# Performance work log

Measured on AMD Instinct MI355X. Metric: run time of the kernel, lower is better.

## Reference

```python
import jax, jax.numpy as jnp
import numpy as np
from jax import lax

K = 16  # neighbors (includes self, as PyG DynamicEdgeConv's knn(x, x, k) does)


def _knn_idx(pts):
    # pts: [n, d] -> [n, K] indices of K nearest points (incl. self)
    sq = jnp.sum(pts * pts, axis=-1)
    dist = sq[:, None] + sq[None, :] - 2.0 * (pts @ pts.T)  # [n, n]
    _, idx = lax.top_k(-dist, K)
    return idx


def _edge_conv(x, w1, b1, w2, b2):
    # x: [B, n, d]. Dynamic kNN in feature space, per-edge MLP, max-aggregation.
    idx = jax.vmap(_knn_idx)(x)                      # [B, n, K]
    xj = jax.vmap(lambda xb, ib: xb[ib])(x, idx)     # [B, n, K, d]
    xi = x[:, :, None, :]
    e = jnp.concatenate([jnp.broadcast_to(xi, xj.shape), xj - xi], axis=-1)  # [B,n,K,2d]
    h = jax.nn.relu(e @ w1 + b1)                     # [B, n, K, h]
    h = h @ w2 + b2                                  # plain last layer (PyG MLP plain_last)
    return jnp.max(h, axis=2)                        # max aggr over neighbors -> [B, n, h]


def setup_inputs() -> dict:
    key = jax.random.key(0)
    ks = jax.random.split(key, 16)
    B, n = 64, 1024
    c1, c2, c3 = 64, 64, 64
    m1, m2, m3, oc = 128, 64, 32, 2

    def lin(k, i, o):
        s = 1.0 / np.sqrt(i)
        return jax.random.uniform(k, (i, o), jnp.float32, -s, s)

    inp = {
        "x": jax.random.normal(ks[0], (B, n, 1), jnp.float32),
        "c1w1": lin(ks[1], 2, c1),   "c1b1": jnp.zeros((c1,), jnp.float32),
        "c1w2": lin(ks[2], c1, c1),  "c1b2": jnp.zeros((c1,), jnp.float32),
        "c2w1": lin(ks[3], 2 * c1, c2), "c2b1": jnp.zeros((c2,), jnp.float32),
        "c2w2": lin(ks[4], c2, c2),  "c2b2": jnp.zeros((c2,), jnp.float32),
        "c3w1": lin(ks[5], 2 * c2, c3), "c3b1": jnp.zeros((c3,), jnp.float32),
        "c3w2": lin(ks[6], c3, c3),  "c3b2": jnp.zeros((c3,), jnp.float32),
        "mw1": lin(ks[7], c1 + c2 + c3, m1), "mb1": jnp.zeros((m1,), jnp.float32),
        "mw2": lin(ks[8], m1, m2),   "mb2": jnp.zeros((m2,), jnp.float32),
        "mw3": lin(ks[9], m2, m3),   "mb3": jnp.zeros((m3,), jnp.float32),
        "mw4": lin(ks[10], m3, oc),  "mb4": jnp.zeros((oc,), jnp.float32),
    }
    return inp


def reference(x, c1w1, c1b1, c1w2, c1b2, c2w1, c2b1, c2w2, c2b2,
              c3w1, c3b1, c3w2, c3b2, mw1, mb1, mw2, mb2, mw3, mb3, mw4, mb4):
    # Three DynamicEdgeConv layers (eval mode: batch-norms are identity at init, dropout off)
    x1 = _edge_conv(x, c1w1, c1b1, c1w2, c1b2)   # [B, n, 64]
    x2 = _edge_conv(x1, c2w1, c2b1, c2w2, c2b2)  # [B, n, 64]
    x3 = _edge_conv(x2, c3w1, c3b1, c3w2, c3b2)  # [B, n, 64]
    h = jnp.concatenate([x1, x2, x3], axis=-1)   # [B, n, 192]
    h = jax.nn.relu(h @ mw1 + mb1)
    h = jax.nn.relu(h @ mw2 + mb2)
    h = jax.nn.relu(h @ mw3 + mb3)
    out = h @ mw4 + mb4                          # [B, n, 2]
    return jax.nn.log_softmax(out, axis=-1)
```

## Files before the change

### kernel.cpp

```cpp
#include <hip/hip_runtime.h>
#include <math.h>

typedef unsigned short ushort_t;
typedef unsigned int uint_t;
typedef unsigned long long u64_t;
typedef __bf16 bf16x8_t __attribute__((ext_vector_type(8)));
typedef float f32x4_t __attribute__((ext_vector_type(4)));

static constexpr int NPTS = 1024;
static constexpr int NB = 64;
static constexpr int NPOINTS = NB * NPTS;
static constexpr int KNB = 16;

__device__ __forceinline__ ushort_t f2bf(float f) {
    uint_t u = __float_as_uint(f);
    uint_t r = (u + 0x7FFFu + ((u >> 16) & 1u)) >> 16;
    return (ushort_t)r;
}
__device__ __forceinline__ uint_t packdj(float d, int j) {
    return (__float_as_uint(fmaxf(d, 0.f)) & 0xFFFFFC00u) | (uint_t)j;
}
__device__ __forceinline__ uint_t med3u(uint_t a, uint_t b, uint_t c) {
    uint_t d;
    asm("v_med3_u32 %0, %1, %2, %3" : "=v"(d) : "v"(a), "v"(b), "v"(c));
    return d;
}
__device__ __forceinline__ void insert16(uint_t* L, uint_t c) {
    #pragma unroll
    for (int k = 15; k > 0; --k)
        L[k] = med3u(L[k - 1], L[k], c);
    L[0] = L[0] < c ? L[0] : c;
}
__device__ __forceinline__ uint_t f2ord(float f) {
    uint_t u = __float_as_uint(f);
    return (u & 0x80000000u) ? ~u : (u ^ 0x80000000u);
}

__global__ __launch_bounds__(256) void prep_kernel(const float* __restrict__ mw1,
                                                   const float* __restrict__ c1w2,
                                                   const float* __restrict__ c2w2,
                                                   const float* __restrict__ c3w2,
                                                   const float* __restrict__ c1w1,
                                                   const float* __restrict__ c1b1,
                                                   const float* __restrict__ c2w1,
                                                   const float* __restrict__ c3w1,
                                                   const float* __restrict__ mw2,
                                                   const float* __restrict__ mw3,
                                                   ushort_t* __restrict__ w1fh,
                                                   ushort_t* __restrict__ w1fl,
                                                   ushort_t* __restrict__ w2fh,
                                                   ushort_t* __restrict__ w2fl,
                                                   float* __restrict__ wuv,
                                                   ushort_t* __restrict__ wuvfh,
                                                   ushort_t* __restrict__ wuvfl,
                                                   ushort_t* __restrict__ w23fh,
                                                   ushort_t* __restrict__ w23fl) {
    int blk = blockIdx.x;
    if (blk < 96) {
        int t = blk * 256 + threadIdx.x;
        int e = t & 7;
        int lane = (t >> 3) & 63;
        int fs = t >> 9;
        int nt = fs / 6, ks = fs - nt * 6;
        int m = lane & 15, quad = lane >> 4;
        int k = ks * 32 + quad * 8 + e;
        int n = nt * 16 + m;
        float w = mw1[k * 128 + n];
        uint_t bits = __float_as_uint(w);
        float hif = __uint_as_float(bits & 0xFFFF0000u);
        w1fh[t] = (ushort_t)(bits >> 16);
        w1fl[t] = f2bf(w - hif);
    } else if (blk < 144) {
        int layer = (blk - 96) >> 4;
        const float* w2 = layer == 0 ? c1w2 : (layer == 1 ? c2w2 : c3w2);
        int t = ((blk - 96) & 15) * 256 + threadIdx.x;
        int e = t & 7;
        int lane = (t >> 3) & 63;
        int fs = t >> 9;
        int ct = fs >> 1, kh = fs & 1;
        int m = lane & 15, quad = lane >> 4;
        int k = kh * 32 + quad * 8 + e;
        int n = ct * 16 + m;
        float w = w2[k * 64 + n];
        uint_t bits = __float_as_uint(w);
        float hif = __uint_as_float(bits & 0xFFFF0000u);
        w2fh[layer * 4096 + t] = (ushort_t)(bits >> 16);
        w2fl[layer * 4096 + t] = f2bf(w - hif);
    } else if (blk == 144) {
        for (int s = threadIdx.x; s < 3072; s += 256) {
            int arr = s >> 10, r = s & 1023;
            int lane = r >> 4, ce = r & 15;
            int kh = ce >> 3, e = ce & 7;
            int quad = lane >> 4;
            int c = kh * 32 + quad * 8 + e;
            float val = (arr == 0) ? (c1w1[c] - c1w1[64 + c])
                      : (arr == 1) ? c1w1[64 + c] : c1b1[c];
            wuv[s] = val;
        }
    } else if (blk < 209) {
        int layer = (blk - 145) >> 5;
        const float* w1 = layer == 0 ? c2w1 : c3w1;
        int t = ((blk - 145) & 31) * 256 + threadIdx.x;
        int e = t & 7;
        int lane = (t >> 3) & 63;
        int fs = t >> 9;
        int nt = fs >> 1, ks = fs & 1;
        int m = lane & 15, quad = lane >> 4;
        int k = ks * 32 + quad * 8 + e;
        float w;
        if (nt < 4) {
            int n = nt * 16 + m;
            w = w1[k * 64 + n] - w1[(64 + k) * 64 + n];
        } else {
            int n = (nt - 4) * 16 + m;
            w = w1[(64 + k) * 64 + n];
        }
        uint_t bits = __float_as_uint(w);
        float hif = __uint_as_float(bits & 0xFFFF0000u);
        wuvfh[layer * 8192 + t] = (ushort_t)(bits >> 16);
        wuvfl[layer * 8192 + t] = f2bf(w - hif);
    } else if (blk < 241) {
        int t = (blk - 209) * 256 + threadIdx.x;
        int e = t & 7;
        int lane = (t >> 3) & 63;
        int fs = t >> 9;
        int nt = fs >> 2, ks = fs & 3;
        int m = lane & 15, quad = lane >> 4;
        int k = ks * 32 + quad * 8 + e;
        int n = nt * 16 + m;
        float w = mw2[k * 64 + n];
        uint_t bits = __float_as_uint(w);
        float hif = __uint_as_float(bits & 0xFFFF0000u);
        w23fh[t] = (ushort_t)(bits >> 16);
        w23fl[t] = f2bf(w - hif);
    } else {
        int t = (blk - 241) * 256 + threadIdx.x;
        int e = t & 7;
        int lane = (t >> 3) & 63;
        int fs = t >> 9;
        int nt = fs >> 1, ks = fs & 1;
        int m = lane & 15, quad = lane >> 4;
        int k = ks * 32 + quad * 8 + e;
        int n = nt * 16 + m;
        float w = mw3[k * 32 + n];
        uint_t bits = __float_as_uint(w);
        float hif = __uint_as_float(bits & 0xFFFF0000u);
        w23fh[8192 + t] = (ushort_t)(bits >> 16);
        w23fl[8192 + t] = f2bf(w - hif);
    }
}

__global__ __launch_bounds__(256) void knn1_sort_kernel(const float* __restrict__ pts,
                                                        int* __restrict__ idx_out) {
    __shared__ u64_t keys[NPTS];
    int b = blockIdx.x;
    int t = threadIdx.x;
    const float* base = pts + (size_t)b * NPTS;
    for (int s = t; s < NPTS; s += 256)
        keys[s] = ((u64_t)f2ord(base[s]) << 32) | (uint_t)s;
    for (int k = 2; k <= NPTS; k <<= 1) {
        for (int j2 = k >> 1; j2 > 0; j2 >>= 1) {
            __syncthreads();
            for (int i = t; i < NPTS; i += 256) {
                int ix = i ^ j2;
                if (ix > i) {
                    bool asc = ((i & k) == 0);
                    u64_t a = keys[i], c = keys[ix];
                    if ((a > c) == asc) { keys[i] = c; keys[ix] = a; }
                }
            }
        }
    }
    __syncthreads();
    for (int s = t; s < NPTS; s += 256) {
        u64_t me = keys[s];
        int jme = (int)(me & 0x3FFu);
        uint_t mo = (uint_t)(me >> 32);
        uint_t mu = (mo & 0x80000000u) ? (mo ^ 0x80000000u) : ~mo;
        float xs = __uint_as_float(mu);
        uint_t lst[KNB];
        #pragma unroll
        for (int k = 0; k < KNB; ++k) lst[k] = 0xFFFFFFFFu;
        int lo = s - 16; if (lo < 0) lo = 0;
        int hi = s + 16; if (hi > NPTS - 1) hi = NPTS - 1;
        for (int q = lo; q <= hi; ++q) {
            u64_t o = keys[q];
            uint_t oo = (uint_t)(o >> 32);
            uint_t ou = (oo & 0x80000000u) ? (oo ^ 0x80000000u) : ~oo;
            float xo = __uint_as_float(ou);
            float d = (xs - xo) * (xs - xo);
            insert16(lst, packdj(d, (int)(o & 0x3FFu)));
        }
        int* op = idx_out + ((size_t)b * NPTS + jme) * KNB;
        #pragma unroll
        for (int k = 0; k < KNB; ++k) op[k] = (int)(lst[k] & 0x3FFu);
    }
}

__global__ __launch_bounds__(256, 4) void knn_mfma_kernel(const ushort_t* __restrict__ xh,
                                                          const ushort_t* __restrict__ xl,
                                                          const float* __restrict__ sq,
                                                          int* __restrict__ idx_out) {
    constexpr int JC = NPTS / 4;
    __shared__ uint_t dmem[4][1088];
    int b    = blockIdx.x & 63;
    int ib   = blockIdx.x >> 6;
    int wave = threadIdx.x >> 6;
    int lane = threadIdx.x & 63;
    int i0   = b * NPTS + ib * 64;
    int m = lane & 15, quad = lane >> 4;
    int j0c = wave * JC;
    uint_t* dbuf = dmem[wave];

    bf16x8_t Ah[4][2], Al[4][2];
    #pragma unroll
    for (int it = 0; it < 4; ++it) {
        #pragma unroll
        for (int kh = 0; kh < 2; ++kh) {
            size_t off = ((size_t)(i0 + it * 16 + m)) * 64 + kh * 32 + quad * 8;
            Ah[it][kh] = *(const bf16x8_t*)(xh + off);
            Al[it][kh] = *(const bf16x8_t*)(xl + off);
        }
    }
    float4 sqi[4];
    #pragma unroll
    for (int it = 0; it < 4; ++it)
        sqi[it] = *(const float4*)&sq[i0 + it * 16 + quad * 4];

    uint_t lst[KNB];
    #pragma unroll
    for (int k = 0; k < KNB; ++k) lst[k] = 0xFFFFFFFFu;

    for (int g = 0; g < JC / 16; ++g) {
        int jg = j0c + g * 16;
        size_t boff = ((size_t)(b * NPTS + jg + m)) * 64 + quad * 8;
        bf16x8_t Bh0 = *(const bf16x8_t*)(xh + boff);
        bf16x8_t Bh1 = *(const bf16x8_t*)(xh + boff + 32);
        bf16x8_t Bl0 = *(const bf16x8_t*)(xl + boff);
        bf16x8_t Bl1 = *(const bf16x8_t*)(xl + boff + 32);
        float sqj = sq[b * NPTS + jg + m];
        int jm = jg + m;
        #pragma unroll
        for (int it = 0; it < 4; ++it) {
            f32x4_t acc = {0.f, 0.f, 0.f, 0.f};
            acc = __builtin_amdgcn_mfma_f32_16x16x32_bf16(Ah[it][0], Bh0, acc, 0, 0, 0);
            acc = __builtin_amdgcn_mfma_f32_16x16x32_bf16(Ah[it][1], Bh1, acc, 0, 0, 0);
            acc = __builtin_amdgcn_mfma_f32_16x16x32_bf16(Ah[it][0], Bl0, acc, 0, 0, 0);
            acc = __builtin_amdgcn_mfma_f32_16x16x32_bf16(Ah[it][1], Bl1, acc, 0, 0, 0);
            acc = __builtin_amdgcn_mfma_f32_16x16x32_bf16(Al[it][0], Bh0, acc, 0, 0, 0);
            acc = __builtin_amdgcn_mfma_f32_16x16x32_bf16(Al[it][1], Bh1, acc, 0, 0, 0);
            uint4 pv;
            pv.x = packdj(sqi[it].x + sqj - 2.0f * acc[0], jm);
            pv.y = packdj(sqi[it].y + sqj - 2.0f * acc[1], jm);
            pv.z = packdj(sqi[it].z + sqj - 2.0f * acc[2], jm);
            pv.w = packdj(sqi[it].w + sqj - 2.0f * acc[3], jm);
            *(uint4*)&dbuf[m * 68 + it * 16 + quad * 4] = pv;
        }
        #pragma unroll
        for (int jj = 0; jj < 16; ++jj)
            insert16(lst, dbuf[jj * 68 + lane]);
    }
    #pragma unroll
    for (int k = 0; k < KNB; ++k) dmem[wave][lane * 17 + k] = lst[k];
    __syncthreads();
    if (wave == 0) {
        uint_t fin[KNB];
        #pragma unroll
        for (int k = 0; k < KNB; ++k) fin[k] = 0xFFFFFFFFu;
        #pragma unroll
        for (int c = 0; c < 4; ++c)
            #pragma unroll
            for (int k = 0; k < KNB; ++k)
                insert16(fin, dmem[c][lane * 17 + k]);
        int* op = idx_out + (size_t)(i0 + lane) * KNB;
        #pragma unroll
        for (int k = 0; k < KNB; ++k) op[k] = (int)(fin[k] & 0x3FFu);
    }
}

__global__ __launch_bounds__(256) void uv_mfma_kernel(const ushort_t* __restrict__ xh,
                                                      const ushort_t* __restrict__ xl,
                                                      const ushort_t* __restrict__ wufh,
                                                      const ushort_t* __restrict__ wufl,
                                                      const float* __restrict__ b1,
                                                      float* __restrict__ u,
                                                      float* __restrict__ v) {
    int wave = threadIdx.x >> 6, lane = threadIdx.x & 63;
    int m = lane & 15, quad = lane >> 4;
    int b = blockIdx.x & 63;
    int r = blockIdx.x >> 6;
    int p0 = b * NPTS + r * 64 + wave * 16;
    bf16x8_t Ah[2], Al[2];
    #pragma unroll
    for (int ks = 0; ks < 2; ++ks) {
        size_t aoff = (size_t)(p0 + m) * 64 + ks * 32 + quad * 8;
        Ah[ks] = *(const bf16x8_t*)(xh + aoff);
        Al[ks] = *(const bf16x8_t*)(xl + aoff);
    }
    f32x4_t acc[8];
    #pragma unroll
    for (int nt = 0; nt < 8; ++nt) acc[nt] = (f32x4_t){0.f, 0.f, 0.f, 0.f};
    #pragma unroll
    for (int ks = 0; ks < 2; ++ks) {
        #pragma unroll
        for (int nt = 0; nt < 8; ++nt) {
            size_t boff = (size_t)((nt * 2 + ks) * 64 + lane) * 8;
            bf16x8_t Bh = *(const bf16x8_t*)(wufh + boff);
            bf16x8_t Bl = *(const bf16x8_t*)(wufl + boff);
            acc[nt] = __builtin_amdgcn_mfma_f32_16x16x32_bf16(Ah[ks], Bh, acc[nt], 0, 0, 0);
            acc[nt] = __builtin_amdgcn_mfma_f32_16x16x32_bf16(Ah[ks], Bl, acc[nt], 0, 0, 0);
            acc[nt] = __builtin_amdgcn_mfma_f32_16x16x32_bf16(Al[ks], Bh, acc[nt], 0, 0, 0);
        }
    }
    #pragma unroll
    for (int nt = 0; nt < 8; ++nt) {
        int ch = (nt & 3) * 16 + m;
        float bb = (nt < 4) ? b1[ch] : 0.f;
        float* dst = (nt < 4) ? u : v;
        #pragma unroll
        for (int rr = 0; rr < 4; ++rr) {
            int p = p0 + quad * 4 + rr;
            dst[(size_t)p * 64 + ch] = acc[nt][rr] + bb;
        }
    }
}

__global__ __launch_bounds__(256) void edge1_mfma_kernel(const float* __restrict__ x0,
                                                         const int* __restrict__ idx,
                                                         const ushort_t* __restrict__ w2fh,
                                                         const ushort_t* __restrict__ w2fl,
                                                         const float* __restrict__ wuv,
                                                         const float* __restrict__ b2,
                                                         ushort_t* __restrict__ oh,
                                                         ushort_t* __restrict__ ol,
                                                         float* __restrict__ sqout) {
    int wave = threadIdx.x >> 6, lane = threadIdx.x & 63;
    int m = lane & 15, quad = lane >> 4;
    bf16x8_t Bh[4][2], Bl[4][2];
    #pragma unroll
    for (int ct = 0; ct < 4; ++ct) {
        #pragma unroll
        for (int kh = 0; kh < 2; ++kh) {
            size_t boff = (size_t)((ct * 2 + kh) * 64 + lane) * 8;
            Bh[ct][kh] = *(const bf16x8_t*)(w2fh + boff);
            Bl[ct][kh] = *(const bf16x8_t*)(w2fl + boff);
        }
    }
    float wdv[16], wbv[16], bbv[16];
    #pragma unroll
    for (int q = 0; q < 4; ++q) {
        *(float4*)&wdv[q * 4] = *(const float4*)&wuv[lane * 16 + q * 4];
        *(float4*)&wbv[q * 4] = *(const float4*)&wuv[1024 + lane * 16 + q * 4];
        *(float4*)&bbv[q * 4] = *(const float4*)&wuv[2048 + lane * 16 + q * 4];
    }
    float bias[4];
    #pragma unroll
    for (int ct = 0; ct < 4; ++ct) bias[ct] = b2[ct * 16 + m];
    int bb_ = blockIdx.x & 63;
    int r_  = blockIdx.x >> 6;
    int p0 = bb_ * NPTS + r_ * 16 + wave * 4;
    int jv[4];
    #pragma unroll
    for (int pi = 0; pi < 4; ++pi) jv[pi] = idx[(p0 + pi) * 16 + m];
    float xj4[4];
    #pragma unroll
    for (int pi = 0; pi < 4; ++pi) xj4[pi] = x0[(bb_ << 10) + jv[pi]];
    #pragma unroll
    for (int pi = 0; pi < 4; ++pi) {
        int p = p0 + pi;
        float xi = x0[p];
        float xj = xj4[pi];
        bf16x8_t Ah[2], Al[2];
        #pragma unroll
        for (int kh = 0; kh < 2; ++kh) {
            union { ushort_t s[8]; bf16x8_t v8; } H, L;
            #pragma unroll
            for (int e = 0; e < 8; ++e) {
                int ce = kh * 8 + e;
                float g = fmaxf(fmaf(xi, wdv[ce], fmaf(xj, wbv[ce], bbv[ce])), 0.f);
                uint_t bits = __float_as_uint(g);
                H.s[e] = (ushort_t)(bits >> 16);
                float hif = __uint_as_float(bits & 0xFFFF0000u);
                L.s[e] = (ushort_t)(__float_as_uint(g - hif) >> 16);
            }
            Ah[kh] = H.v8; Al[kh] = L.v8;
        }
        float val[4];
        #pragma unroll
        for (int ct = 0; ct < 4; ++ct) {
            f32x4_t acc = {0.f, 0.f, 0.f, 0.f};
            acc = __builtin_amdgcn_mfma_f32_16x16x32_bf16(Ah[0], Bh[ct][0], acc, 0, 0, 0);
            acc = __builtin_amdgcn_mfma_f32_16x16x32_bf16(Ah[1], Bh[ct][1], acc, 0, 0, 0);
            acc = __builtin_amdgcn_mfma_f32_16x16x32_bf16(Ah[0], Bl[ct][0], acc, 0, 0, 0);
            acc = __builtin_amdgcn_mfma_f32_16x16x32_bf16(Ah[1], Bl[ct][1], acc, 0, 0, 0);
            acc = __builtin_amdgcn_mfma_f32_16x16x32_bf16(Al[0], Bh[ct][0], acc, 0, 0, 0);
            acc = __builtin_amdgcn_mfma_f32_16x16x32_bf16(Al[1], Bh[ct][1], acc, 0, 0, 0);
            float mm = fmaxf(fmaxf(acc[0], acc[1]), fmaxf(acc[2], acc[3]));
            mm = fmaxf(mm, __shfl_xor(mm, 16, 64));
            mm = fmaxf(mm, __shfl_xor(mm, 32, 64));
            val[ct] = mm + bias[ct];
        }
        {
            float partial = val[0] * val[0] + val[1] * val[1]
                          + val[2] * val[2] + val[3] * val[3];
            partial += __shfl_xor(partial, 1, 64);
            partial += __shfl_xor(partial, 2, 64);
            partial += __shfl_xor(partial, 4, 64);
            partial += __shfl_xor(partial, 8, 64);
            if (lane == 0) sqout[p] = partial;
        }
        if (quad == 0) {
            #pragma unroll
            for (int ct = 0; ct < 4; ++ct) {
                int o = ct * 16 + m;
                float vv = val[ct];
                uint_t bits = __float_as_uint(vv);
                oh[(size_t)p * 64 + o] = (ushort_t)(bits >> 16);
                float hif = __uint_as_float(bits & 0xFFFF0000u);
                ol[(size_t)p * 64 + o] = f2bf(vv - hif);
            }
        }
    }
}

template<bool WSQ>
__global__ __launch_bounds__(256) void edge_mfma_kernel(const float* __restrict__ u,
                                                        const float* __restrict__ v,
                                                        const int* __restrict__ idx,
                                                        const ushort_t* __restrict__ w2fh,
                                                        const ushort_t* __restrict__ w2fl,
                                                        const float* __restrict__ b2,
                                                        ushort_t* __restrict__ oh,
                                                        ushort_t* __restrict__ ol,
                                                        float* __restrict__ sqout) {
    int wave = threadIdx.x >> 6, lane = threadIdx.x & 63;
    int m = lane & 15, quad = lane >> 4;
    bf16x8_t Bh[4][2], Bl[4][2];
    #pragma unroll
    for (int ct = 0; ct < 4; ++ct) {
        #pragma unroll
        for (int kh = 0; kh < 2; ++kh) {
            size_t boff = (size_t)((ct * 2 + kh) * 64 + lane) * 8;
            Bh[ct][kh] = *(const bf16x8_t*)(w2fh + boff);
            Bl[ct][kh] = *(const bf16x8_t*)(w2fl + boff);
        }
    }
    float bias[4];
    #pragma unroll
    for (int ct = 0; ct < 4; ++ct) bias[ct] = b2[ct * 16 + m];
    int bb_ = blockIdx.x & 63;
    int r_  = blockIdx.x >> 6;
    int p0 = bb_ * NPTS + r_ * 16 + wave * 4;
    int jv[4];
    #pragma unroll
    for (int pi = 0; pi < 4; ++pi) jv[pi] = idx[(p0 + pi) * 16 + m];
    #pragma unroll
    for (int pi = 0; pi < 4; ++pi) {
        int p = p0 + pi;
        const float* up = u + (size_t)p * 64;
        const float* vp = v + ((size_t)(bb_ << 10) + jv[pi]) * 64;
        bf16x8_t Ah[2], Al[2];
        #pragma unroll
        for (int kh = 0; kh < 2; ++kh) {
            int c0 = kh * 32 + quad * 8;
            float4 ua = *(const float4*)(up + c0);
            float4 ub = *(const float4*)(up + c0 + 4);
            float4 va = *(const float4*)(vp + c0);
            float4 vb = *(const float4*)(vp + c0 + 4);
            float f[8] = {ua.x + va.x, ua.y + va.y, ua.z + va.z, ua.w + va.w,
                          ub.x + vb.x, ub.y + vb.y, ub.z + vb.z, ub.w + vb.w};
            union { ushort_t s[8]; bf16x8_t v8; } H, L;
            #pragma unroll
            for (int e = 0; e < 8; ++e) {
                float g = fmaxf(f[e], 0.f);
                uint_t bits = __float_as_uint(g);
                H.s[e] = (ushort_t)(bits >> 16);
                float hif = __uint_as_float(bits & 0xFFFF0000u);
                L.s[e] = (ushort_t)(__float_as_uint(g - hif) >> 16);
            }
            Ah[kh] = H.v8; Al[kh] = L.v8;
        }
        float val[4];
        #pragma unroll
        for (int ct = 0; ct < 4; ++ct) {
            f32x4_t acc = {0.f, 0.f, 0.f, 0.f};
            acc = __builtin_amdgcn_mfma_f32_16x16x32_bf16(Ah[0], Bh[ct][0], acc, 0, 0, 0);
            acc = __builtin_amdgcn_mfma_f32_16x16x32_bf16(Ah[1], Bh[ct][1], acc, 0, 0, 0);
            acc = __builtin_amdgcn_mfma_f32_16x16x32_bf16(Ah[0], Bl[ct][0], acc, 0, 0, 0);
            acc = __builtin_amdgcn_mfma_f32_16x16x32_bf16(Ah[1], Bl[ct][1], acc, 0, 0, 0);
            acc = __builtin_amdgcn_mfma_f32_16x16x32_bf16(Al[0], Bh[ct][0], acc, 0, 0, 0);
            acc = __builtin_amdgcn_mfma_f32_16x16x32_bf16(Al[1], Bh[ct][1], acc, 0, 0, 0);
            float mm = fmaxf(fmaxf(acc[0], acc[1]), fmaxf(acc[2], acc[3]));
            mm = fmaxf(mm, __shfl_xor(mm, 16, 64));
            mm = fmaxf(mm, __shfl_xor(mm, 32, 64));
            val[ct] = mm + bias[ct];
        }
        if constexpr (WSQ) {
            float partial = val[0] * val[0] + val[1] * val[1]
                          + val[2] * val[2] + val[3] * val[3];
            partial += __shfl_xor(partial, 1, 64);
            partial += __shfl_xor(partial, 2, 64);
            partial += __shfl_xor(partial, 4, 64);
            partial += __shfl_xor(partial, 8, 64);
            if (lane == 0) sqout[p] = partial;
        }
        if (quad == 0) {
            #pragma unroll
            for (int ct = 0; ct < 4; ++ct) {
                int o = ct * 16 + m;
                float vv = val[ct];
                uint_t bits = __float_as_uint(vv);
                oh[(size_t)p * 64 + o] = (ushort_t)(bits >> 16);
                float hif = __uint_as_float(bits & 0xFFFF0000u);
                ol[(size_t)p * 64 + o] = f2bf(vv - hif);
            }
        }
    }
}

__global__ __launch_bounds__(128, 2) void mlp_kernel(const ushort_t* __restrict__ xh1,
                                                  const ushort_t* __restrict__ xl1,
                                                  const ushort_t* __restrict__ xh2,
                                                  const ushort_t* __restrict__ xl2,
                                                  const ushort_t* __restrict__ xh3,
                                                  const ushort_t* __restrict__ xl3,
                                                  const ushort_t* __restrict__ w1fh,
                                                  const ushort_t* __restrict__ w1fl,
                                                  const ushort_t* __restrict__ w23fh,
                                                  const ushort_t* __restrict__ w23fl,
                                                  const float* __restrict__ mb1,
                                                  const float* __restrict__ mb2,
                                                  const float* __restrict__ mb3,
                                                  const float* __restrict__ mw4, const float* __restrict__ mb4,
                                                  float* __restrict__ out) {
    __shared__ float smem[2][128 * 17];
    int wave = threadIdx.x >> 6, lane = threadIdx.x & 63;
    float* h1w = smem[wave];
    float* h2w = smem[wave];
    float* h3w = smem[wave] + 64 * 17;
    int m = lane & 15, quad = lane >> 4;
    int pw = blockIdx.x * 32 + wave * 16;

    const ushort_t* HS[3] = {xh1, xh2, xh3};
    const ushort_t* LS[3] = {xl1, xl2, xl3};
    bf16x8_t Ah[6], Al[6];
    #pragma unroll
    for (int ks = 0; ks < 6; ++ks) {
        size_t aoff = (size_t)(pw + m) * 64 + (ks & 1) * 32 + quad * 8;
        Ah[ks] = *(const bf16x8_t*)(HS[ks >> 1] + aoff);
        Al[ks] = *(const bf16x8_t*)(LS[ks >> 1] + aoff);
    }
    f32x4_t acc1[8];
    #pragma unroll
    for (int nt = 0; nt < 8; ++nt) acc1[nt] = (f32x4_t){0.f, 0.f, 0.f, 0.f};
    #pragma unroll
    for (int ks = 0; ks < 6; ++ks) {
        bf16x8_t Bh[8], Bl[8];
        #pragma unroll
        for (int nt = 0; nt < 8; ++nt) {
            size_t boff = (size_t)(nt * 6 + ks) * 512 + lane * 8;
            Bh[nt] = *(const bf16x8_t*)(w1fh + boff);
            Bl[nt] = *(const bf16x8_t*)(w1fl + boff);
        }
        #pragma unroll
        for (int nt = 0; nt < 8; ++nt) {
            acc1[nt] = __builtin_amdgcn_mfma_f32_16x16x32_bf16(Ah[ks], Bh[nt], acc1[nt], 0, 0, 0);
            acc1[nt] = __builtin_amdgcn_mfma_f32_16x16x32_bf16(Ah[ks], Bl[nt], acc1[nt], 0, 0, 0);
            acc1[nt] = __builtin_amdgcn_mfma_f32_16x16x32_bf16(Al[ks], Bh[nt], acc1[nt], 0, 0, 0);
        }
    }
    #pragma unroll
    for (int nt = 0; nt < 8; ++nt) {
        float bb = mb1[nt * 16 + m];
        float4 w;
        w.x = fmaxf(acc1[nt][0] + bb, 0.f);
        w.y = fmaxf(acc1[nt][1] + bb, 0.f);
        w.z = fmaxf(acc1[nt][2] + bb, 0.f);
        w.w = fmaxf(acc1[nt][3] + bb, 0.f);
        *(float4*)&h1w[(nt * 16 + m) * 17 + quad * 4] = w;
    }
    f32x4_t acc2[4];
    #pragma unroll
    for (int nt = 0; nt < 4; ++nt) acc2[nt] = (f32x4_t){0.f, 0.f, 0.f, 0.f};
    #pragma unroll
    for (int ks = 0; ks < 4; ++ks) {
        union { ushort_t s[8]; bf16x8_t v8; } H, L;
        #pragma unroll
        for (int e = 0; e < 8; ++e) {
            float g = h1w[(ks * 32 + quad * 8 + e) * 17 + m];
            uint_t bits = __float_as_uint(g);
            H.s[e] = (ushort_t)(bits >> 16);
            float hif = __uint_as_float(bits & 0xFFFF0000u);
            L.s[e] = f2bf(g - hif);
        }
        bf16x8_t A2h = H.v8, A2l = L.v8;
        #pragma unroll
        for (int nt = 0; nt < 4; ++nt) {
            size_t boff = (size_t)(nt * 4 + ks) * 512 + lane * 8;
            bf16x8_t Bh = *(const bf16x8_t*)(w23fh + boff);
            bf16x8_t Bl = *(const bf16x8_t*)(w23fl + boff);
            acc2[nt] = __builtin_amdgcn_mfma_f32_16x16x32_bf16(A2h, Bh, acc2[nt], 0, 0, 0);
            acc2[nt] = __builtin_amdgcn_mfma_f32_16x16x32_bf16(A2h, Bl, acc2[nt], 0, 0, 0);
            acc2[nt] = __builtin_amdgcn_mfma_f32_16x16x32_bf16(A2l, Bh, acc2[nt], 0, 0, 0);
        }
    }
    #pragma unroll
    for (int nt = 0; nt < 4; ++nt) {
        float bb = mb2[nt * 16 + m];
        float4 w;
        w.x = fmaxf(acc2[nt][0] + bb, 0.f);
        w.y = fmaxf(acc2[nt][1] + bb, 0.f);
        w.z = fmaxf(acc2[nt][2] + bb, 0.f);
        w.w = fmaxf(acc2[nt][3] + bb, 0.f);
        *(float4*)&h2w[(nt * 16 + m) * 17 + quad * 4] = w;
    }
    f32x4_t acc3[2];
    #pragma unroll
    for (int nt = 0; nt < 2; ++nt) acc3[nt] = (f32x4_t){0.f, 0.f, 0.f, 0.f};
    #pragma unroll
    for (int ks = 0; ks < 2; ++ks) {
        union { ushort_t s[8]; bf16x8_t v8; } H, L;
        #pragma unroll
        for (int e = 0; e < 8; ++e) {
            float g = h2w[(ks * 32 + quad * 8 + e) * 17 + m];
            uint_t bits = __float_as_uint(g);
            H.s[e] = (ushort_t)(bits >> 16);
            float hif = __uint_as_float(bits & 0xFFFF0000u);
            L.s[e] = f2bf(g - hif);
        }
        bf16x8_t A3h = H.v8, A3l = L.v8;
        #pragma unroll
        for (int nt = 0; nt < 2; ++nt) {
            size_t boff = (size_t)(8192 + (nt * 2 + ks) * 512) + lane * 8;
            bf16x8_t Bh = *(const bf16x8_t*)(w23fh + boff);
            bf16x8_t Bl = *(const bf16x8_t*)(w23fl + boff);
            acc3[nt] = __builtin_amdgcn_mfma_f32_16x16x32_bf16(A3h, Bh, acc3[nt], 0, 0, 0);
            acc3[nt] = __builtin_amdgcn_mfma_f32_16x16x32_bf16(A3h, Bl, acc3[nt], 0, 0, 0);
            acc3[nt] = __builtin_amdgcn_mfma_f32_16x16x32_bf16(A3l, Bh, acc3[nt], 0, 0, 0);
        }
    }
    #pragma unroll
    for (int nt = 0; nt < 2; ++nt) {
        float bb = mb3[nt * 16 + m];
        float4 w;
        w.x = fmaxf(acc3[nt][0] + bb, 0.f);
        w.y = fmaxf(acc3[nt][1] + bb, 0.f);
        w.z = fmaxf(acc3[nt][2] + bb, 0.f);
        w.w = fmaxf(acc3[nt][3] + bb, 0.f);
        *(float4*)&h3w[(nt * 16 + m) * 17 + quad * 4] = w;
    }
    if (lane < 16) {
        float z0 = mb4[0], z1 = mb4[1];
        #pragma unroll 8
        for (int c = 0; c < 32; ++c) {
            float h = h3w[c * 17 + lane];
            z0 = fmaf(h, mw4[c * 2 + 0], z0);
            z1 = fmaf(h, mw4[c * 2 + 1], z1);
        }
        float mx = fmaxf(z0, z1);
        float ls = mx + logf(expf(z0 - mx) + expf(z1 - mx));
        float2 o; o.x = z0 - ls; o.y = z1 - ls;
        *(float2*)&out[(size_t)(pw + lane) * 2] = o;
    }
}

extern "C" void kernel_launch(void* const* d_in, const int* in_sizes, int n_in,
                              void* d_out, int out_size, void* d_ws, size_t ws_size,
                              hipStream_t stream) {
    const float* x0   = (const float*)d_in[0];
    const float* c1w1 = (const float*)d_in[1];  const float* c1b1 = (const float*)d_in[2];
    const float* c1w2 = (const float*)d_in[3];  const float* c1b2 = (const float*)d_in[4];
    const float* c2w1 = (const float*)d_in[5];  const float* c2b1 = (const float*)d_in[6];
    const float* c2w2 = (const float*)d_in[7];  const float* c2b2 = (const float*)d_in[8];
    const float* c3w1 = (const float*)d_in[9];  const float* c3b1 = (const float*)d_in[10];
    const float* c3w2 = (const float*)d_in[11]; const float* c3b2 = (const float*)d_in[12];
    const float* mw1  = (const float*)d_in[13]; const float* mb1  = (const float*)d_in[14];
    const float* mw2  = (const float*)d_in[15]; const float* mb2  = (const float*)d_in[16];
    const float* mw3  = (const float*)d_in[17]; const float* mb3  = (const float*)d_in[18];
    const float* mw4  = (const float*)d_in[19]; const float* mb4  = (const float*)d_in[20];

    float* ws = (float*)d_ws;
    const size_t NF = (size_t)NPOINTS * 64;
    float* u  = ws;
    float* v  = u + NF;
    float* sq = v + NF;
    int*  idx = (int*)(sq + NPOINTS);
    ushort_t* xh1 = (ushort_t*)(idx + (size_t)NPOINTS * KNB);
    ushort_t* xl1 = xh1 + NF;
    ushort_t* xh2 = xl1 + NF;
    ushort_t* xl2 = xh2 + NF;
    ushort_t* xh3 = xl2 + NF;
    ushort_t* xl3 = xh3 + NF;
    ushort_t* w1fh = xl3 + NF;
    ushort_t* w1fl = w1fh + 128 * 192;
    ushort_t* w2fh = w1fl + 128 * 192;
    ushort_t* w2fl = w2fh + 3 * 4096;
    float* wuv = (float*)(w2fl + 3 * 4096);
    ushort_t* wuvfh = (ushort_t*)(wuv + 3072);
    ushort_t* wuvfl = wuvfh + 2 * 8192;
    ushort_t* w23fh = wuvfl + 2 * 8192;
    ushort_t* w23fl = w23fh + 10240;
    float* out = (float*)d_out;

    prep_kernel<<<249, 256, 0, stream>>>(mw1, c1w2, c2w2, c3w2, c1w1, c1b1,
                                         c2w1, c3w1, mw2, mw3,
                                         w1fh, w1fl, w2fh, w2fl,
                                         wuv, wuvfh, wuvfl, w23fh, w23fl);
    knn1_sort_kernel<<<NB, 256, 0, stream>>>(x0, idx);
    edge1_mfma_kernel<<<NB * 64, 256, 0, stream>>>(
        x0, idx, w2fh, w2fl, wuv, c1b2, xh1, xl1, sq);
    knn_mfma_kernel<<<NB * 16, 256, 0, stream>>>(xh1, xl1, sq, idx);
    uv_mfma_kernel<<<NB * 16, 256, 0, stream>>>(xh1, xl1, wuvfh, wuvfl, c2b1, u, v);
    edge_mfma_kernel<true><<<NPOINTS / 16, 256, 0, stream>>>(
        u, v, idx, w2fh + 4096, w2fl + 4096, c2b2, xh2, xl2, sq);
    knn_mfma_kernel<<<NB * 16, 256, 0, stream>>>(xh2, xl2, sq, idx);
    uv_mfma_kernel<<<NB * 16, 256, 0, stream>>>(xh2, xl2, wuvfh + 8192, wuvfl + 8192,
                                                c3b1, u, v);
    edge_mfma_kernel<false><<<NPOINTS / 16, 256, 0, stream>>>(
        u, v, idx, w2fh + 8192, w2fl + 8192, c3b2, xh3, xl3, nullptr);
    mlp_kernel<<<NPOINTS / 32, 128, 0, stream>>>(xh1, xl1, xh2, xl2, xh3, xl3,
                                                 w1fh, w1fl, w23fh, w23fl,
                                                 mb1, mb2, mb3, mw4, mb4, out);
}
```

Before: 485.9 us.

## Split kNN candidate range across two blocks and merge partial top-16 lists

The kNN kernel now splits the 1024 candidate points of each query tile across two blocks (512 each) and doubles the grid, so more blocks run concurrently and each wave's serial insertion loop is half as long. Each block writes its packed partial top-16 keys to a scratch buffer, and a new merge kernel combines the two lists per point into the final indices. It also stages squared norms in shared memory. The costs are an extra launch, extra global traffic for the partial lists, and a duplicated per-block final merge. The scratch buffer sits after the existing workspace, which assumes that allocation is large enough.

```diff
diff --git a/kernel.cpp b/kernel.cpp
--- a/kernel.cpp
+++ b/kernel.cpp
@@ -200,17 +200,22 @@
 __global__ __launch_bounds__(256, 4) void knn_mfma_kernel(const ushort_t* __restrict__ xh,
                                                           const ushort_t* __restrict__ xl,
                                                           const float* __restrict__ sq,
-                                                          int* __restrict__ idx_out) {
-    constexpr int JC = NPTS / 4;
+                                                          uint_t* __restrict__ pout) {
+    constexpr int JC = 128;
     __shared__ uint_t dmem[4][1088];
+    __shared__ float sqs[4][JC];
     int b    = blockIdx.x & 63;
-    int ib   = blockIdx.x >> 6;
+    int r    = blockIdx.x >> 6;
+    int ib   = r & 15;
+    int jh   = r >> 4;
     int wave = threadIdx.x >> 6;
     int lane = threadIdx.x & 63;
     int i0   = b * NPTS + ib * 64;
     int m = lane & 15, quad = lane >> 4;
-    int j0c = wave * JC;
+    int j0c = jh * 512 + wave * JC;
     uint_t* dbuf = dmem[wave];
+
+    for (int t = lane; t < JC; t += 64) sqs[wave][t] = sq[b * NPTS + j0c + t];
 
     bf16x8_t Ah[4][2], Al[4][2];
     #pragma unroll
@@ -238,7 +243,7 @@
         bf16x8_t Bh1 = *(const bf16x8_t*)(xh + boff + 32);
         bf16x8_t Bl0 = *(const bf16x8_t*)(xl + boff);
         bf16x8_t Bl1 = *(const bf16x8_t*)(xl + boff + 32);
-        float sqj = sq[b * NPTS + jg + m];
+        float sqj = sqs[wave][g * 16 + m];
         int jm = jg + m;
         #pragma unroll
         for (int it = 0; it < 4; ++it) {
@@ -272,10 +277,33 @@
             #pragma unroll
             for (int k = 0; k < KNB; ++k)
                 insert16(fin, dmem[c][lane * 17 + k]);
-        int* op = idx_out + (size_t)(i0 + lane) * KNB;
-        #pragma unroll
-        for (int k = 0; k < KNB; ++k) op[k] = (int)(fin[k] & 0x3FFu);
-    }
+        uint_t* op = pout + ((size_t)jh * NPOINTS + i0 + lane) * KNB;
+        #pragma unroll
+        for (int k = 0; k < KNB; ++k) op[k] = fin[k];
+    }
+}
+
+__global__ __launch_bounds__(256) void knn_merge_kernel(const uint_t* __restrict__ pknn,
+                                                        int* __restrict__ idx_out) {
+    int p = blockIdx.x * 256 + threadIdx.x;
+    union { uint4 v[4]; uint_t s[16]; } A, B;
+    const uint4* ap = (const uint4*)(pknn + (size_t)p * KNB);
+    const uint4* bp = (const uint4*)(pknn + ((size_t)NPOINTS + p) * KNB);
+    #pragma unroll
+    for (int q = 0; q < 4; ++q) A.v[q] = ap[q];
+    #pragma unroll
+    for (int q = 0; q < 4; ++q) B.v[q] = bp[q];
+    uint_t lst[KNB];
+    #pragma unroll
+    for (int k = 0; k < KNB; ++k) lst[k] = A.s[k];
+    #pragma unroll
+    for (int k = 0; k < KNB; ++k) insert16(lst, B.s[k]);
+    union { int4 v[4]; int s[16]; } O;
+    #pragma unroll
+    for (int k = 0; k < KNB; ++k) O.s[k] = (int)(lst[k] & 0x3FFu);
+    int4* op = (int4*)(idx_out + (size_t)p * KNB);
+    #pragma unroll
+    for (int q = 0; q < 4; ++q) op[q] = O.v[q];
 }
 
 __global__ __launch_bounds__(256) void uv_mfma_kernel(const ushort_t* __restrict__ xh,
@@ -700,6 +728,7 @@
     ushort_t* wuvfl = wuvfh + 2 * 8192;
     ushort_t* w23fh = wuvfl + 2 * 8192;
     ushort_t* w23fl = w23fh + 10240;
+    uint_t* pknn = (uint_t*)(w23fl + 10240);
     float* out = (float*)d_out;
 
     prep_kernel<<<249, 256, 0, stream>>>(mw1, c1w2, c2w2, c3w2, c1w1, c1b1,
@@ -709,11 +738,13 @@
     knn1_sort_kernel<<<NB, 256, 0, stream>>>(x0, idx);
     edge1_mfma_kernel<<<NB * 64, 256, 0, stream>>>(
         x0, idx, w2fh, w2fl, wuv, c1b2, xh1, xl1, sq);
-    knn_mfma_kernel<<<NB * 16, 256, 0, stream>>>(xh1, xl1, sq, idx);
+    knn_mfma_kernel<<<NB * 32, 256, 0, stream>>>(xh1, xl1, sq, pknn);
+    knn_merge_kernel<<<NPOINTS / 256, 256, 0, stream>>>(pknn, idx);
     uv_mfma_kernel<<<NB * 16, 256, 0, stream>>>(xh1, xl1, wuvfh, wuvfl, c2b1, u, v);
     edge_mfma_kernel<true><<<NPOINTS / 16, 256, 0, stream>>>(
         u, v, idx, w2fh + 4096, w2fl + 4096, c2b2, xh2, xl2, sq);
-    knn_mfma_kernel<<<NB * 16, 256, 0, stream>>>(xh2, xl2, sq, idx);
+    knn_mfma_kernel<<<NB * 32, 256, 0, stream>>>(xh2, xl2, sq, pknn);
+    knn_merge_kernel<<<NPOINTS / 256, 256, 0, stream>>>(pknn, idx);
     uv_mfma_kernel<<<NB * 16, 256, 0, stream>>>(xh2, xl2, wuvfh + 8192, wuvfl + 8192,
                                                 c3b1, u, v);
     edge_mfma_kernel<false><<<NPOINTS / 16, 256, 0, stream>>>(
```

Result: slower. 506.8 us (+4.3%).

## Restructure kNN MFMA kernel: per-wave query rows, register top-k with shuffle merge

Applied to the files above, without the earlier changes.

Each wave now owns 16 query points and sweeps all 1024 candidates, swapping MFMA operand roles so every lane holds four distances for its own query row. Lanes insert those distances straight into a register top-16 list instead of going through the shared-memory transpose buffer. The four lane-groups' partial lists are then merged with xor shuffles instead of a block-level LDS merge and __syncthreads. This removes LDS traffic and the barrier, at the cost of more global loads of candidate rows per wave and more insert16 calls per lane.

```diff
diff --git a/kernel.cpp b/kernel.cpp
--- a/kernel.cpp
+++ b/kernel.cpp
@@ -201,80 +201,72 @@
                                                           const ushort_t* __restrict__ xl,
                                                           const float* __restrict__ sq,
                                                           int* __restrict__ idx_out) {
-    constexpr int JC = NPTS / 4;
-    __shared__ uint_t dmem[4][1088];
     int b    = blockIdx.x & 63;
-    int ib   = blockIdx.x >> 6;
+    int r    = blockIdx.x >> 6;
     int wave = threadIdx.x >> 6;
     int lane = threadIdx.x & 63;
-    int i0   = b * NPTS + ib * 64;
     int m = lane & 15, quad = lane >> 4;
-    int j0c = wave * JC;
-    uint_t* dbuf = dmem[wave];
-
-    bf16x8_t Ah[4][2], Al[4][2];
-    #pragma unroll
-    for (int it = 0; it < 4; ++it) {
-        #pragma unroll
-        for (int kh = 0; kh < 2; ++kh) {
-            size_t off = ((size_t)(i0 + it * 16 + m)) * 64 + kh * 32 + quad * 8;
-            Ah[it][kh] = *(const bf16x8_t*)(xh + off);
-            Al[it][kh] = *(const bf16x8_t*)(xl + off);
-        }
-    }
-    float4 sqi[4];
-    #pragma unroll
-    for (int it = 0; it < 4; ++it)
-        sqi[it] = *(const float4*)&sq[i0 + it * 16 + quad * 4];
+    int it = r * 4 + wave;
+    int i0 = b * NPTS + it * 16;
+
+    bf16x8_t Bih[2], Bil[2];
+    #pragma unroll
+    for (int kh = 0; kh < 2; ++kh) {
+        size_t off = (size_t)(i0 + m) * 64 + kh * 32 + quad * 8;
+        Bih[kh] = *(const bf16x8_t*)(xh + off);
+        Bil[kh] = *(const bf16x8_t*)(xl + off);
+    }
+    float sqi = sq[i0 + m];
 
     uint_t lst[KNB];
     #pragma unroll
     for (int k = 0; k < KNB; ++k) lst[k] = 0xFFFFFFFFu;
 
-    for (int g = 0; g < JC / 16; ++g) {
-        int jg = j0c + g * 16;
-        size_t boff = ((size_t)(b * NPTS + jg + m)) * 64 + quad * 8;
-        bf16x8_t Bh0 = *(const bf16x8_t*)(xh + boff);
-        bf16x8_t Bh1 = *(const bf16x8_t*)(xh + boff + 32);
-        bf16x8_t Bl0 = *(const bf16x8_t*)(xl + boff);
-        bf16x8_t Bl1 = *(const bf16x8_t*)(xl + boff + 32);
-        float sqj = sq[b * NPTS + jg + m];
-        int jm = jg + m;
-        #pragma unroll
-        for (int it = 0; it < 4; ++it) {
-            f32x4_t acc = {0.f, 0.f, 0.f, 0.f};
-            acc = __builtin_amdgcn_mfma_f32_16x16x32_bf16(Ah[it][0], Bh0, acc, 0, 0, 0);
-            acc = __builtin_amdgcn_mfma_f32_16x16x32_bf16(Ah[it][1], Bh1, acc, 0, 0, 0);
-            acc = __builtin_amdgcn_mfma_f32_16x16x32_bf16(Ah[it][0], Bl0, acc, 0, 0, 0);
-            acc = __builtin_amdgcn_mfma_f32_16x16x32_bf16(Ah[it][1], Bl1, acc, 0, 0, 0);
-            acc = __builtin_amdgcn_mfma_f32_16x16x32_bf16(Al[it][0], Bh0, acc, 0, 0, 0);
-            acc = __builtin_amdgcn_mfma_f32_16x16x32_bf16(Al[it][1], Bh1, acc, 0, 0, 0);
-            uint4 pv;
-            pv.x = packdj(sqi[it].x + sqj - 2.0f * acc[0], jm);
-            pv.y = packdj(sqi[it].y + sqj - 2.0f * acc[1], jm);
-            pv.z = packdj(sqi[it].z + sqj - 2.0f * acc[2], jm);
-            pv.w = packdj(sqi[it].w + sqj - 2.0f * acc[3], jm);
-            *(uint4*)&dbuf[m * 68 + it * 16 + quad * 4] = pv;
-        }
-        #pragma unroll
-        for (int jj = 0; jj < 16; ++jj)
-            insert16(lst, dbuf[jj * 68 + lane]);
-    }
-    #pragma unroll
-    for (int k = 0; k < KNB; ++k) dmem[wave][lane * 17 + k] = lst[k];
-    __syncthreads();
-    if (wave == 0) {
-        uint_t fin[KNB];
-        #pragma unroll
-        for (int k = 0; k < KNB; ++k) fin[k] = 0xFFFFFFFFu;
-        #pragma unroll
-        for (int c = 0; c < 4; ++c)
-            #pragma unroll
-            for (int k = 0; k < KNB; ++k)
-                insert16(fin, dmem[c][lane * 17 + k]);
-        int* op = idx_out + (size_t)(i0 + lane) * KNB;
-        #pragma unroll
-        for (int k = 0; k < KNB; ++k) op[k] = (int)(fin[k] & 0x3FFu);
+    #pragma unroll 2
+    for (int g = 0; g < 64; ++g) {
+        int jg = g * 16;
+        size_t aoff = (size_t)(b * NPTS + jg + m) * 64 + quad * 8;
+        bf16x8_t Ah0 = *(const bf16x8_t*)(xh + aoff);
+        bf16x8_t Ah1 = *(const bf16x8_t*)(xh + aoff + 32);
+        bf16x8_t Al0 = *(const bf16x8_t*)(xl + aoff);
+        bf16x8_t Al1 = *(const bf16x8_t*)(xl + aoff + 32);
+        float4 sqj = *(const float4*)&sq[b * NPTS + jg + quad * 4];
+        f32x4_t acc = {0.f, 0.f, 0.f, 0.f};
+        acc = __builtin_amdgcn_mfma_f32_16x16x32_bf16(Ah0, Bih[0], acc, 0, 0, 0);
+        acc = __builtin_amdgcn_mfma_f32_16x16x32_bf16(Ah1, Bih[1], acc, 0, 0, 0);
+        acc = __builtin_amdgcn_mfma_f32_16x16x32_bf16(Ah0, Bil[0], acc, 0, 0, 0);
+        acc = __builtin_amdgcn_mfma_f32_16x16x32_bf16(Ah1, Bil[1], acc, 0, 0, 0);
+        acc = __builtin_amdgcn_mfma_f32_16x16x32_bf16(Al0, Bih[0], acc, 0, 0, 0);
+        acc = __builtin_amdgcn_mfma_f32_16x16x32_bf16(Al1, Bih[1], acc, 0, 0, 0);
+        int j0 = jg + quad * 4;
+        insert16(lst, packdj(fmaf(-2.0f, acc[0], sqi + sqj.x), j0));
+        insert16(lst, packdj(fmaf(-2.0f, acc[1], sqi + sqj.y), j0 + 1));
+        insert16(lst, packdj(fmaf(-2.0f, acc[2], sqi + sqj.z), j0 + 2));
+        insert16(lst, packdj(fmaf(-2.0f, acc[3], sqi + sqj.w), j0 + 3));
+    }
+    uint_t tmp[KNB];
+    #pragma unroll
+    for (int k = 0; k < KNB; ++k) tmp[k] = __shfl_xor(lst[k], 16, 64);
+    #pragma unroll
+    for (int k = 0; k < KNB; ++k) insert16(lst, tmp[k]);
+    #pragma unroll
+    for (int k = 0; k < KNB; ++k) tmp[k] = __shfl_xor(lst[k], 32, 64);
+    #pragma unroll
+    for (int k = 0; k < KNB; ++k) insert16(lst, tmp[k]);
+    if (quad == 0) {
+        int* op = idx_out + (size_t)(i0 + m) * KNB;
+        int4 o0 = {(int)(lst[0] & 0x3FFu), (int)(lst[1] & 0x3FFu),
+                   (int)(lst[2] & 0x3FFu), (int)(lst[3] & 0x3FFu)};
+        int4 o1 = {(int)(lst[4] & 0x3FFu), (int)(lst[5] & 0x3FFu),
+                   (int)(lst[6] & 0x3FFu), (int)(lst[7] & 0x3FFu)};
+        int4 o2 = {(int)(lst[8] & 0x3FFu), (int)(lst[9] & 0x3FFu),
+                   (int)(lst[10] & 0x3FFu), (int)(lst[11] & 0x3FFu)};
+        int4 o3 = {(int)(lst[12] & 0x3FFu), (int)(lst[13] & 0x3FFu),
+                   (int)(lst[14] & 0x3FFu), (int)(lst[15] & 0x3FFu)};
+        *(int4*)(op + 0)  = o0;
+        *(int4*)(op + 4)  = o1;
+        *(int4*)(op + 8)  = o2;
+        *(int4*)(op + 12) = o3;
     }
 }
 
```

Result: slower. 601.9 us (+23.9%).

## Fuse kNN and UV projection into one launch; merge partial top-k lists bitonically

Applied to the files above, without the earlier changes.

The kNN and u/v projection kernels become a single launch in which even blocks do kNN and odd blocks do the projection. This removes a kernel launch per layer and lets the lightweight projection blocks fill gaps while the heavy kNN blocks run. The kNN path now stages squared norms of the candidate points in shared memory. The final reduction of the four per-wave top-16 lists uses a bitonic merge instead of 64 serial insertions. Mixing roles in one grid may give uneven block scheduling, and the extra shared memory could affect occupancy.

```diff
diff --git a/kernel.cpp b/kernel.cpp
--- a/kernel.cpp
+++ b/kernel.cpp
@@ -30,6 +30,24 @@
     for (int k = 15; k > 0; --k)
         L[k] = med3u(L[k - 1], L[k], c);
     L[0] = L[0] < c ? L[0] : c;
+}
+__device__ __forceinline__ void merge16(uint_t* L, const uint_t* B) {
+    uint_t t[16];
+    #pragma unroll
+    for (int k = 0; k < 16; ++k) t[k] = L[k] < B[15 - k] ? L[k] : B[15 - k];
+    #pragma unroll
+    for (int j = 8; j >= 1; j >>= 1) {
+        #pragma unroll
+        for (int k = 0; k < 16; ++k) {
+            if ((k & j) == 0) {
+                uint_t a = t[k], c = t[k | j];
+                t[k] = a < c ? a : c;
+                t[k | j] = a < c ? c : a;
+            }
+        }
+    }
+    #pragma unroll
+    for (int k = 0; k < 16; ++k) L[k] = t[k];
 }
 __device__ __forceinline__ uint_t f2ord(float f) {
     uint_t u = __float_as_uint(f);
@@ -197,130 +215,132 @@
     }
 }
 
-__global__ __launch_bounds__(256, 4) void knn_mfma_kernel(const ushort_t* __restrict__ xh,
-                                                          const ushort_t* __restrict__ xl,
-                                                          const float* __restrict__ sq,
-                                                          int* __restrict__ idx_out) {
-    constexpr int JC = NPTS / 4;
+__global__ __launch_bounds__(256, 4) void knnuv_kernel(const ushort_t* __restrict__ xh,
+                                                       const ushort_t* __restrict__ xl,
+                                                       const float* __restrict__ sq,
+                                                       int* __restrict__ idx_out,
+                                                       const ushort_t* __restrict__ wufh,
+                                                       const ushort_t* __restrict__ wufl,
+                                                       const float* __restrict__ b1,
+                                                       float* __restrict__ u,
+                                                       float* __restrict__ v) {
     __shared__ uint_t dmem[4][1088];
-    int b    = blockIdx.x & 63;
-    int ib   = blockIdx.x >> 6;
+    __shared__ float sqs[4][256];
+    int role = blockIdx.x & 1;
+    int id   = blockIdx.x >> 1;
     int wave = threadIdx.x >> 6;
     int lane = threadIdx.x & 63;
-    int i0   = b * NPTS + ib * 64;
     int m = lane & 15, quad = lane >> 4;
-    int j0c = wave * JC;
-    uint_t* dbuf = dmem[wave];
-
-    bf16x8_t Ah[4][2], Al[4][2];
-    #pragma unroll
-    for (int it = 0; it < 4; ++it) {
-        #pragma unroll
-        for (int kh = 0; kh < 2; ++kh) {
-            size_t off = ((size_t)(i0 + it * 16 + m)) * 64 + kh * 32 + quad * 8;
-            Ah[it][kh] = *(const bf16x8_t*)(xh + off);
-            Al[it][kh] = *(const bf16x8_t*)(xl + off);
-        }
-    }
-    float4 sqi[4];
-    #pragma unroll
-    for (int it = 0; it < 4; ++it)
-        sqi[it] = *(const float4*)&sq[i0 + it * 16 + quad * 4];
-
-    uint_t lst[KNB];
-    #pragma unroll
-    for (int k = 0; k < KNB; ++k) lst[k] = 0xFFFFFFFFu;
-
-    for (int g = 0; g < JC / 16; ++g) {
-        int jg = j0c + g * 16;
-        size_t boff = ((size_t)(b * NPTS + jg + m)) * 64 + quad * 8;
-        bf16x8_t Bh0 = *(const bf16x8_t*)(xh + boff);
-        bf16x8_t Bh1 = *(const bf16x8_t*)(xh + boff + 32);
-        bf16x8_t Bl0 = *(const bf16x8_t*)(xl + boff);
-        bf16x8_t Bl1 = *(const bf16x8_t*)(xl + boff + 32);
-        float sqj = sq[b * NPTS + jg + m];
-        int jm = jg + m;
+
+    if (role == 0) {
+        constexpr int JC = NPTS / 4;
+        int b  = id & 63;
+        int ib = id >> 6;
+        int i0 = b * NPTS + ib * 64;
+        int j0c = wave * JC;
+        uint_t* dbuf = dmem[wave];
+
+        for (int t = lane; t < JC; t += 64) sqs[wave][t] = sq[b * NPTS + j0c + t];
+
+        bf16x8_t Ah[4][2], Al[4][2];
         #pragma unroll
         for (int it = 0; it < 4; ++it) {
-            f32x4_t acc = {0.f, 0.f, 0.f, 0.f};
-            acc = __builtin_amdgcn_mfma_f32_16x16x32_bf16(Ah[it][0], Bh0, acc, 0, 0, 0);
-            acc = __builtin_amdgcn_mfma_f32_16x16x32_bf16(Ah[it][1], Bh1, acc, 0, 0, 0);
-            acc = __builtin_amdgcn_mfma_f32_16x16x32_bf16(Ah[it][0], Bl0, acc, 0, 0, 0);
-            acc = __builtin_amdgcn_mfma_f32_16x16x32_bf16(Ah[it][1], Bl1, acc, 0, 0, 0);
-            acc = __builtin_amdgcn_mfma_f32_16x16x32_bf16(Al[it][0], Bh0, acc, 0, 0, 0);
-            acc = __builtin_amdgcn_mfma_f32_16x16x32_bf16(Al[it][1], Bh1, acc, 0, 0, 0);
-            uint4 pv;
-            pv.x = packdj(sqi[it].x + sqj - 2.0f * acc[0], jm);
-            pv.y = packdj(sqi[it].y + sqj - 2.0f * acc[1], jm);
-            pv.z = packdj(sqi[it].z + sqj - 2.0f * acc[2], jm);
-            pv.w = packdj(sqi[it].w + sqj - 2.0f * acc[3], jm);
-            *(uint4*)&dbuf[m * 68 + it * 16 + quad * 4] = pv;
-        }
-        #pragma unroll
-        for (int jj = 0; jj < 16; ++jj)
-            insert16(lst, dbuf[jj * 68 + lane]);
-    }
-    #pragma unroll
-    for (int k = 0; k < KNB; ++k) dmem[wave][lane * 17 + k] = lst[k];
-    __syncthreads();
-    if (wave == 0) {
-        uint_t fin[KNB];
-        #pragma unroll
-        for (int k = 0; k < KNB; ++k) fin[k] = 0xFFFFFFFFu;
-        #pragma unroll
-        for (int c = 0; c < 4; ++c)
-            #pragma unroll
-            for (int k = 0; k < KNB; ++k)
-                insert16(fin, dmem[c][lane * 17 + k]);
-        int* op = idx_out + (size_t)(i0 + lane) * KNB;
-        #pragma unroll
-        for (int k = 0; k < KNB; ++k) op[k] = (int)(fin[k] & 0x3FFu);
-    }
-}
-
-__global__ __launch_bounds__(256) void uv_mfma_kernel(const ushort_t* __restrict__ xh,
-                                                      const ushort_t* __restrict__ xl,
-                                                      const ushort_t* __restrict__ wufh,
-                                                      const ushort_t* __restrict__ wufl,
-                                                      const float* __restrict__ b1,
-                                                      float* __restrict__ u,
-                                                      float* __restrict__ v) {
-    int wave = threadIdx.x >> 6, lane = threadIdx.x & 63;
-    int m = lane & 15, quad = lane >> 4;
-    int b = blockIdx.x & 63;
-    int r = blockIdx.x >> 6;
-    int p0 = b * NPTS + r * 64 + wave * 16;
-    bf16x8_t Ah[2], Al[2];
-    #pragma unroll
-    for (int ks = 0; ks < 2; ++ks) {
-        size_t aoff = (size_t)(p0 + m) * 64 + ks * 32 + quad * 8;
-        Ah[ks] = *(const bf16x8_t*)(xh + aoff);
-        Al[ks] = *(const bf16x8_t*)(xl + aoff);
-    }
-    f32x4_t acc[8];
-    #pragma unroll
-    for (int nt = 0; nt < 8; ++nt) acc[nt] = (f32x4_t){0.f, 0.f, 0.f, 0.f};
-    #pragma unroll
-    for (int ks = 0; ks < 2; ++ks) {
+            #pragma unroll
+            for (int kh = 0; kh < 2; ++kh) {
+                size_t off = ((size_t)(i0 + it * 16 + m)) * 64 + kh * 32 + quad * 8;
+                Ah[it][kh] = *(const bf16x8_t*)(xh + off);
+                Al[it][kh] = *(const bf16x8_t*)(xl + off);
+            }
+        }
+        float4 sqi[4];
+        #pragma unroll
+        for (int it = 0; it < 4; ++it)
+            sqi[it] = *(const float4*)&sq[i0 + it * 16 + quad * 4];
+
+        uint_t lst[KNB];
+        #pragma unroll
+        for (int k = 0; k < KNB; ++k) lst[k] = 0xFFFFFFFFu;
+
+        for (int g = 0; g < JC / 16; ++g) {
+            int jg = j0c + g * 16;
+            size_t boff = ((size_t)(b * NPTS + jg + m)) * 64 + quad * 8;
+            bf16x8_t Bh0 = *(const bf16x8_t*)(xh + boff);
+            bf16x8_t Bh1 = *(const bf16x8_t*)(xh + boff + 32);
+            bf16x8_t Bl0 = *(const bf16x8_t*)(xl + boff);
+            bf16x8_t Bl1 = *(const bf16x8_t*)(xl + boff + 32);
+            float sqj = sqs[wave][g * 16 + m];
+            int jm = jg + m;
+            #pragma unroll
+            for (int it = 0; it < 4; ++it) {
+                f32x4_t acc = {0.f, 0.f, 0.f, 0.f};
+                acc = __builtin_amdgcn_mfma_f32_16x16x32_bf16(Ah[it][0], Bh0, acc, 0, 0, 0);
+                acc = __builtin_amdgcn_mfma_f32_16x16x32_bf16(Ah[it][1], Bh1, acc, 0, 0, 0);
+                acc = __builtin_amdgcn_mfma_f32_16x16x32_bf16(Ah[it][0], Bl0, acc, 0, 0, 0);
+                acc = __builtin_amdgcn_mfma_f32_16x16x32_bf16(Ah[it][1], Bl1, acc, 0, 0, 0);
+                acc = __builtin_amdgcn_mfma_f32_16x16x32_bf16(Al[it][0], Bh0, acc, 0, 0, 0);
+                acc = __builtin_amdgcn_mfma_f32_16x16x32_bf16(Al[it][1], Bh1, acc, 0, 0, 0);
+                uint4 pv;
+                pv.x = packdj(sqi[it].x + sqj - 2.0f * acc[0], jm);
+                pv.y = packdj(sqi[it].y + sqj - 2.0f * acc[1], jm);
+                pv.z = packdj(sqi[it].z + sqj - 2.0f * acc[2], jm);
+                pv.w = packdj(sqi[it].w + sqj - 2.0f * acc[3], jm);
+                *(uint4*)&dbuf[m * 68 + it * 16 + quad * 4] = pv;
+            }
+            #pragma unroll
+            for (int jj = 0; jj < 16; ++jj)
+                insert16(lst, dbuf[jj * 68 + lane]);
+        }
+        #pragma unroll
+        for (int k = 0; k < KNB; ++k) dmem[wave][lane * 17 + k] = lst[k];
+        __syncthreads();
+        if (wave == 0) {
+            uint_t bl[KNB];
+            #pragma unroll
+            for (int c = 1; c < 4; ++c) {
+                #pragma unroll
+                for (int k = 0; k < KNB; ++k) bl[k] = dmem[c][lane * 17 + k];
+                merge16(lst, bl);
+            }
+            int* op = idx_out + (size_t)(i0 + lane) * KNB;
+            #pragma unroll
+            for (int k = 0; k < KNB; ++k) op[k] = (int)(lst[k] & 0x3FFu);
+        }
+    } else {
+        int b = id & 63;
+        int r = id >> 6;
+        int p0 = b * NPTS + r * 64 + wave * 16;
+        bf16x8_t Ah[2], Al[2];
+        #pragma unroll
+        for (int ks = 0; ks < 2; ++ks) {
+            size_t aoff = (size_t)(p0 + m) * 64 + ks * 32 + quad * 8;
+            Ah[ks] = *(const bf16x8_t*)(xh + aoff);
+            Al[ks] = *(const bf16x8_t*)(xl + aoff);
+        }
+        f32x4_t acc[8];
+        #pragma unroll
+        for (int nt = 0; nt < 8; ++nt) acc[nt] = (f32x4_t){0.f, 0.f, 0.f, 0.f};
+        #pragma unroll
+        for (int ks = 0; ks < 2; ++ks) {
+            #pragma unroll
+            for (int nt = 0; nt < 8; ++nt) {
+                size_t boff = (size_t)((nt * 2 + ks) * 64 + lane) * 8;
+                bf16x8_t Bh = *(const bf16x8_t*)(wufh + boff);
+                bf16x8_t Bl = *(const bf16x8_t*)(wufl + boff);
+                acc[nt] = __builtin_amdgcn_mfma_f32_16x16x32_bf16(Ah[ks], Bh, acc[nt], 0, 0, 0);
+                acc[nt] = __builtin_amdgcn_mfma_f32_16x16x32_bf16(Ah[ks], Bl, acc[nt], 0, 0, 0);
+                acc[nt] = __builtin_amdgcn_mfma_f32_16x16x32_bf16(Al[ks], Bh, acc[nt], 0, 0, 0);
+            }
+        }
         #pragma unroll
         for (int nt = 0; nt < 8; ++nt) {
-            size_t boff = (size_t)((nt * 2 + ks) * 64 + lane) * 8;
-            bf16x8_t Bh = *(const bf16x8_t*)(wufh + boff);
-            bf16x8_t Bl = *(const bf16x8_t*)(wufl + boff);
-            acc[nt] = __builtin_amdgcn_mfma_f32_16x16x32_bf16(Ah[ks], Bh, acc[nt], 0, 0, 0);
-            acc[nt] = __builtin_amdgcn_mfma_f32_16x16x32_bf16(Ah[ks], Bl, acc[nt], 0, 0, 0);
-            acc[nt] = __builtin_amdgcn_mfma_f32_16x16x32_bf16(Al[ks], Bh, acc[nt], 0, 0, 0);
-        }
-    }
-    #pragma unroll
-    for (int nt = 0; nt < 8; ++nt) {
-        int ch = (nt & 3) * 16 + m;
-        float bb = (nt < 4) ? b1[ch] : 0.f;
-        float* dst = (nt < 4) ? u : v;
-        #pragma unroll
-        for (int rr = 0; rr < 4; ++rr) {
-            int p = p0 + quad * 4 + rr;
-            dst[(size_t)p * 64 + ch] = acc[nt][rr] + bb;
+            int ch = (nt & 3) * 16 + m;
+            float bb = (nt < 4) ? b1[ch] : 0.f;
+            float* dst = (nt < 4) ? u : v;
+            #pragma unroll
+            for (int rr = 0; rr < 4; ++rr) {
+                int p = p0 + quad * 4 + rr;
+                dst[(size_t)p * 64 + ch] = acc[nt][rr] + bb;
+            }
         }
     }
 }
@@ -709,13 +729,12 @@
     knn1_sort_kernel<<<NB, 256, 0, stream>>>(x0, idx);
     edge1_mfma_kernel<<<NB * 64, 256, 0, stream>>>(
         x0, idx, w2fh, w2fl, wuv, c1b2, xh1, xl1, sq);
-    knn_mfma_kernel<<<NB * 16, 256, 0, stream>>>(xh1, xl1, sq, idx);
-    uv_mfma_kernel<<<NB * 16, 256, 0, stream>>>(xh1, xl1, wuvfh, wuvfl, c2b1, u, v);
+    knnuv_kernel<<<2048, 256, 0, stream>>>(xh1, xl1, sq, idx,
+                                           wuvfh, wuvfl, c2b1, u, v);
     edge_mfma_kernel<true><<<NPOINTS / 16, 256, 0, stream>>>(
         u, v, idx, w2fh + 4096, w2fl + 4096, c2b2, xh2, xl2, sq);
-    knn_mfma_kernel<<<NB * 16, 256, 0, stream>>>(xh2, xl2, sq, idx);
-    uv_mfma_kernel<<<NB * 16, 256, 0, stream>>>(xh2, xl2, wuvfh + 8192, wuvfl + 8192,
-                                                c3b1, u, v);
+    knnuv_kernel<<<2048, 256, 0, stream>>>(xh2, xl2, sq, idx,
+                                           wuvfh + 8192, wuvfl + 8192, c3b1, u, v);
     edge_mfma_kernel<false><<<NPOINTS / 16, 256, 0, stream>>>(
         u, v, idx, w2fh + 8192, w2fl + 8192, c3b2, xh3, xl3, nullptr);
     mlp_kernel<<<NPOINTS / 32, 128, 0, stream>>>(xh1, xl1, xh2, xl2, xh3, xl3,
```

After: 541.6 us. 11.5% more time.
